# Kernel optimization log

Hardware: AMD Instinct MI355X
Metric: run time of the kernel (lower is better)

Reference implementation:

```python
import jax, jax.numpy as jnp
import numpy as np

EPS = 1e-5
NUM_HEADS = 16
HEAD_DIM = 64


def layernorm(x, g, b):
    mu = jnp.mean(x, axis=-1, keepdims=True)
    var = jnp.mean(jnp.square(x - mu), axis=-1, keepdims=True)
    return (x - mu) * jax.lax.rsqrt(var + EPS) * g + b


def setup_inputs() -> dict:
    key = jax.random.key(0)
    ks = jax.random.split(key, 10)
    B, S, Q, D = 4, 4096, 256, 1024
    x = jax.random.normal(ks[0], (B, S, D), dtype=jnp.float32)
    queries = jax.random.normal(ks[1], (B, Q, D), dtype=jnp.float32)
    attn_mask = jax.random.randint(ks[2], (B, NUM_HEADS, Q, S), 0, 2) == 1
    key_padding_mask = jax.random.randint(ks[3], (B, S), 0, 2) == 1
    scale = 1.0 / np.sqrt(2.0 * D)  # xavier-ish
    Wq = jax.random.normal(ks[4], (D, D), dtype=jnp.float32) * scale
    Wk = jax.random.normal(ks[5], (D, D), dtype=jnp.float32) * scale
    Wv = jax.random.normal(ks[6], (D, D), dtype=jnp.float32) * scale
    Wo = jax.random.normal(ks[7], (D, D), dtype=jnp.float32) * scale
    ln1_g = jnp.ones((D,), jnp.float32); ln1_b = jnp.zeros((D,), jnp.float32)
    ln2_g = jnp.ones((D,), jnp.float32); ln2_b = jnp.zeros((D,), jnp.float32)
    return {"x": x, "queries": queries, "attn_mask": attn_mask,
            "key_padding_mask": key_padding_mask, "Wq": Wq, "Wk": Wk,
            "Wv": Wv, "Wo": Wo, "ln1_g": ln1_g, "ln1_b": ln1_b,
            "ln2_g": ln2_g, "ln2_b": ln2_b}


def reference(x, queries, attn_mask, key_padding_mask, Wq, Wk, Wv, Wo,
              ln1_g, ln1_b, ln2_g, ln2_b):
    B, S, D = x.shape
    Q = queries.shape[1]
    H, hd = NUM_HEADS, HEAD_DIM

    xn = layernorm(x, ln1_g, ln1_b)
    q = (queries @ Wq.T).reshape(B, Q, H, hd)
    k = (xn @ Wk.T).reshape(B, S, H, hd)
    v = (xn @ Wv.T).reshape(B, S, H, hd)

    # scores: (B, H, Q, S)
    scores = jnp.einsum('bqhd,bshd->bhqs', q, k) / np.sqrt(hd)

    mask = attn_mask | key_padding_mask[:, None, None, :]
    neg_inf = jnp.float32(-jnp.inf)
    masked = jnp.where(mask, neg_inf, scores)
    all_masked = jnp.all(mask, axis=-1, keepdims=True)  # rows fully masked
    safe = jnp.where(all_masked, 0.0, masked)
    attn = jax.nn.softmax(safe, axis=-1)
    attn = jnp.where(all_masked, 0.0, attn)

    out = jnp.einsum('bhqs,bshd->bqhd', attn, v).reshape(B, Q, D)
    out = layernorm(out, ln2_g, ln2_b)
    return out @ Wo.T, attn.mean(axis=1)
```

## Files before the change

kernel.cpp:

```cpp
#include <hip/hip_runtime.h>
#include <math.h>

#define DEV __device__ __forceinline__

typedef float  f4v  __attribute__((ext_vector_type(4)));
typedef __bf16 b8v  __attribute__((ext_vector_type(8)));
typedef short  s8v  __attribute__((ext_vector_type(8)));

DEV short f2b(float f){ __bf16 h = (__bf16)f; return __builtin_bit_cast(short, h); }

DEV void gload16(const void* g, void* l){
  __builtin_amdgcn_global_load_lds((const __attribute__((address_space(1))) void*)g,
                                   (__attribute__((address_space(3))) void*)l, 16, 0, 0);
}

DEV b8v ldsf(const short* p){ return __builtin_bit_cast(b8v, *(const s8v*)p); }

DEV f4v mfma16(b8v a, b8v b, f4v c){ return __builtin_amdgcn_mfma_f32_16x16x32_bf16(a, b, c, 0, 0, 0); }

__global__ void cvt5_kernel(const float* __restrict__ s0, const float* __restrict__ s1,
                            const float* __restrict__ s2, const float* __restrict__ s3,
                            const float* __restrict__ s4,
                            short* __restrict__ d0, short* __restrict__ d1,
                            short* __restrict__ d2, short* __restrict__ d3,
                            short* __restrict__ d4){
  int i = blockIdx.x*256 + threadIdx.x;
  int buf = i >> 18, j = i & 262143;
  const float* s = (buf==0)?s0:(buf==1)?s1:(buf==2)?s2:(buf==3)?s3:s4;
  short*       d = (buf==0)?d0:(buf==1)?d1:(buf==2)?d2:(buf==3)?d3:d4;
  float4 v = ((const float4*)s)[j];
  ((short4*)d)[j] = make_short4(f2b(v.x), f2b(v.y), f2b(v.z), f2b(v.w));
}

__global__ __launch_bounds__(256) void ln_kernel(const float* __restrict__ x, const float* __restrict__ gg,
                                                 const float* __restrict__ bb, short* __restrict__ out){
  int row = blockIdx.x, tid = threadIdx.x;
  const float4 v = ((const float4*)(x + (size_t)row*1024))[tid];
  float s = v.x + v.y + v.z + v.w;
  #pragma unroll
  for (int off=1; off<64; off<<=1) s += __shfl_xor(s, off);
  __shared__ float red[4];
  if ((tid&63)==0) red[tid>>6] = s;
  __syncthreads();
  float mu = (red[0]+red[1]+red[2]+red[3]) * (1.0f/1024.0f);
  float d0=v.x-mu, d1=v.y-mu, d2=v.z-mu, d3=v.w-mu;
  float q = d0*d0 + d1*d1 + d2*d2 + d3*d3;
  #pragma unroll
  for (int off=1; off<64; off<<=1) q += __shfl_xor(q, off);
  __syncthreads();
  if ((tid&63)==0) red[tid>>6] = q;
  __syncthreads();
  float rs = rsqrtf((red[0]+red[1]+red[2]+red[3]) * (1.0f/1024.0f) + 1e-5f);
  float4 g4 = ((const float4*)gg)[tid];
  float4 b4 = ((const float4*)bb)[tid];
  short4 o = make_short4(f2b(d0*rs*g4.x + b4.x), f2b(d1*rs*g4.y + b4.y),
                         f2b(d2*rs*g4.z + b4.z), f2b(d3*rs*g4.w + b4.w));
  ((short4*)(out + (size_t)row*1024))[tid] = o;
}

__global__ __launch_bounds__(256) void ln_reduce_kernel(const float* __restrict__ opart, const float* __restrict__ gg,
                                                        const float* __restrict__ bb, short* __restrict__ out){
  int row = blockIdx.x, tid = threadIdx.x;
  float4 v = make_float4(0.f,0.f,0.f,0.f);
  #pragma unroll
  for (int sc=0; sc<16; ++sc){
    float4 t = ((const float4*)(opart + ((size_t)sc*1024 + row)*1024))[tid];
    v.x += t.x; v.y += t.y; v.z += t.z; v.w += t.w;
  }
  float s = v.x + v.y + v.z + v.w;
  #pragma unroll
  for (int off=1; off<64; off<<=1) s += __shfl_xor(s, off);
  __shared__ float red[4];
  if ((tid&63)==0) red[tid>>6] = s;
  __syncthreads();
  float mu = (red[0]+red[1]+red[2]+red[3]) * (1.0f/1024.0f);
  float d0=v.x-mu, d1=v.y-mu, d2=v.z-mu, d3=v.w-mu;
  float q = d0*d0 + d1*d1 + d2*d2 + d3*d3;
  #pragma unroll
  for (int off=1; off<64; off<<=1) q += __shfl_xor(q, off);
  __syncthreads();
  if ((tid&63)==0) red[tid>>6] = q;
  __syncthreads();
  float rs = rsqrtf((red[0]+red[1]+red[2]+red[3]) * (1.0f/1024.0f) + 1e-5f);
  float4 g4 = ((const float4*)gg)[tid];
  float4 b4 = ((const float4*)bb)[tid];
  short4 o = make_short4(f2b(d0*rs*g4.x + b4.x), f2b(d1*rs*g4.y + b4.y),
                         f2b(d2*rs*g4.z + b4.z), f2b(d3*rs*g4.w + b4.w));
  ((short4*)(out + (size_t)row*1024))[tid] = o;
}

template<int OUTF32>
__global__ __launch_bounds__(256,2) void gemm_bt(const short* __restrict__ A, const short* __restrict__ B,
                                                 void* __restrict__ C, int M, int N, int K){
  __shared__ short sA[128*32];
  __shared__ short sB[128*32];
  int tid=threadIdx.x, lane=tid&63, wv=tid>>6, g=lane>>4, r=lane&15;
  int wr=wv>>1, wc=wv&1;
  int m0=blockIdx.x*128, n0=blockIdx.y*128;
  f4v z = {0.f,0.f,0.f,0.f};
  f4v acc[4][4];
  #pragma unroll
  for (int i=0;i<4;++i){
    #pragma unroll
    for (int j=0;j<4;++j) acc[i][j]=z;
  }
  int nkt = K >> 5;
  for (int kt=0; kt<nkt; ++kt){
    __syncthreads();
    #pragma unroll
    for (int i=0;i<2;++i){
      int idx = i*256 + wv*64 + lane;
      int row = idx>>2, sl = idx&3;
      gload16(A + (size_t)(m0+row)*K + kt*32 + sl*8, &sA[(i*256+wv*64)*8]);
    }
    #pragma unroll
    for (int i=0;i<2;++i){
      int idx = i*256 + wv*64 + lane;
      int row = idx>>2, sl = idx&3;
      gload16(B + (size_t)(n0+row)*K + kt*32 + sl*8, &sB[(i*256+wv*64)*8]);
    }
    __syncthreads();
    b8v af[4], bf[4];
    #pragma unroll
    for (int mf=0;mf<4;++mf) af[mf] = ldsf(&sA[(wr*64+mf*16+r)*32 + g*8]);
    #pragma unroll
    for (int nf=0;nf<4;++nf) bf[nf] = ldsf(&sB[(wc*64+nf*16+r)*32 + g*8]);
    #pragma unroll
    for (int mf=0;mf<4;++mf){
      #pragma unroll
      for (int nf=0;nf<4;++nf)
        acc[mf][nf] = mfma16(af[mf], bf[nf], acc[mf][nf]);
    }
  }
  #pragma unroll
  for (int mf=0;mf<4;++mf){
    #pragma unroll
    for (int nf=0;nf<4;++nf){
      #pragma unroll
      for (int j=0;j<4;++j){
        int m = m0 + wr*64 + mf*16 + g*4 + j;
        int n = n0 + wc*64 + nf*16 + r;
        if (OUTF32) ((float*)C)[(size_t)m*N + n] = acc[mf][nf][j];
        else        ((short*)C)[(size_t)m*N + n] = f2b(acc[mf][nf][j]);
      }
    }
  }
}

__global__ __launch_bounds__(512,2) void gemm_dual_bt(const short* __restrict__ A, const short* __restrict__ B0,
                                                      const short* __restrict__ B1, short* __restrict__ C0,
                                                      short* __restrict__ C1, int M, int N, int K){
  __shared__ short sA[256*32];
  __shared__ short sB0[128*32];
  __shared__ short sB1[128*32];
  int tid=threadIdx.x, lane=tid&63, wv=tid>>6, g=lane>>4, r=lane&15;
  int wr=wv>>1, wc=wv&1;
  int m0=blockIdx.x*256, n0=blockIdx.y*128;
  f4v z = {0.f,0.f,0.f,0.f};
  f4v a0[4][4], a1[4][4];
  #pragma unroll
  for (int i=0;i<4;++i){
    #pragma unroll
    for (int j=0;j<4;++j){ a0[i][j]=z; a1[i][j]=z; }
  }
  int nkt = K >> 5;
  for (int kt=0; kt<nkt; ++kt){
    __syncthreads();
    #pragma unroll
    for (int i=0;i<2;++i){
      int idx = i*512 + tid;
      int row = idx>>2, sl = idx&3;
      gload16(A + (size_t)(m0+row)*K + kt*32 + sl*8, &sA[(i*512+wv*64)*8]);
    }
    {
      int row = tid>>2, sl = tid&3;
      gload16(B0 + (size_t)(n0+row)*K + kt*32 + sl*8, &sB0[(wv*64)*8]);
      gload16(B1 + (size_t)(n0+row)*K + kt*32 + sl*8, &sB1[(wv*64)*8]);
    }
    __syncthreads();
    b8v af[4], b0[4], b1[4];
    #pragma unroll
    for (int mf=0;mf<4;++mf) af[mf] = ldsf(&sA[(wr*64+mf*16+r)*32 + g*8]);
    #pragma unroll
    for (int nf=0;nf<4;++nf){
      b0[nf] = ldsf(&sB0[(wc*64+nf*16+r)*32 + g*8]);
      b1[nf] = ldsf(&sB1[(wc*64+nf*16+r)*32 + g*8]);
    }
    #pragma unroll
    for (int mf=0;mf<4;++mf){
      #pragma unroll
      for (int nf=0;nf<4;++nf){
        a0[mf][nf] = mfma16(af[mf], b0[nf], a0[mf][nf]);
        a1[mf][nf] = mfma16(af[mf], b1[nf], a1[mf][nf]);
      }
    }
  }
  #pragma unroll
  for (int mf=0;mf<4;++mf){
    #pragma unroll
    for (int nf=0;nf<4;++nf){
      #pragma unroll
      for (int j=0;j<4;++j){
        int m = m0 + wr*64 + mf*16 + g*4 + j;
        int n = n0 + wc*64 + nf*16 + r;
        C0[(size_t)m*N + n] = f2b(a0[mf][nf][j]);
        C1[(size_t)m*N + n] = f2b(a1[mf][nf][j]);
      }
    }
  }
}

__global__ __launch_bounds__(256) void vtrans_kernel(const short* __restrict__ v, short* __restrict__ vt){
  int bid = blockIdx.x;
  int sb = bid & 63, bh = bid >> 6;
  int b = bh >> 4, h = bh & 15;
  int s0 = sb*64;
  __shared__ short t[64][80];
  int tid = threadIdx.x;
  #pragma unroll
  for (int i=0;i<2;++i){
    int idx = tid + i*256;
    int row = idx>>3, sl = idx&7;
    *(s8v*)&t[row][sl*8] = *(const s8v*)(v + (size_t)(b*4096 + s0 + row)*1024 + h*64 + sl*8);
  }
  __syncthreads();
  int hd = tid>>2, part = tid&3;
  s8v o0, o1;
  #pragma unroll
  for (int j=0;j<8;++j){ o0[j] = t[part*16+j][hd]; o1[j] = t[part*16+8+j][hd]; }
  size_t base = (size_t)(bh*64+hd)*4096 + s0 + part*16;
  *(s8v*)(vt + base)     = o0;
  *(s8v*)(vt + base + 8) = o1;
}

__global__ __launch_bounds__(256,2) void lsum_kernel(const short* __restrict__ qp, const short* __restrict__ kb,
                                                     const int* __restrict__ am, const int* __restrict__ kpm,
                                                     unsigned* __restrict__ pm, float* __restrict__ lpart){
  int bid = blockIdx.x;
  int sc = bid & 15, bh = bid >> 4;
  int b = bh >> 4, h = bh & 15;
  int s0 = sc*256;
  __shared__ short sQ[256*64];
  __shared__ short sK[256*64];
  __shared__ unsigned sPM[256*8];
  __shared__ unsigned kw[8];
  int tid=threadIdx.x, lane=tid&63, wv=tid>>6, g=lane>>4, r=lane&15;

  #pragma unroll
  for (int i=0;i<8;++i){
    int idx = i*256 + wv*64 + lane;
    int row = idx>>3, cbs = (idx&7)^(row&7);
    gload16(qp + (size_t)(b*256 + row)*1024 + h*64 + cbs*8, &sQ[(i*256+wv*64)*8]);
  }
  #pragma unroll
  for (int i=0;i<8;++i){
    int idx = i*256 + wv*64 + lane;
    int row = idx>>3, cbs = (idx&7)^(row&7);
    gload16(kb + (size_t)(b*4096 + s0 + row)*1024 + h*64 + cbs*8, &sK[(i*256+wv*64)*8]);
  }
  if (tid < 8){
    unsigned bits = 0;
    const int4* kp = (const int4*)(kpm + (size_t)b*4096 + s0 + tid*32);
    #pragma unroll
    for (int j=0;j<8;++j){
      int4 t = kp[j];
      bits |= (unsigned)(t.x!=0) << (j*4+0);
      bits |= (unsigned)(t.y!=0) << (j*4+1);
      bits |= (unsigned)(t.z!=0) << (j*4+2);
      bits |= (unsigned)(t.w!=0) << (j*4+3);
    }
    kw[tid] = bits;
  }
  unsigned rowbits[8];
  const int4* ap = (const int4*)(am + (size_t)(bh*256 + tid)*4096 + s0);
  #pragma unroll
  for (int w=0;w<8;++w){
    unsigned bits = 0;
    #pragma unroll
    for (int j=0;j<8;++j){
      int4 t = ap[w*8+j];
      bits |= (unsigned)(t.x!=0) << (j*4+0);
      bits |= (unsigned)(t.y!=0) << (j*4+1);
      bits |= (unsigned)(t.z!=0) << (j*4+2);
      bits |= (unsigned)(t.w!=0) << (j*4+3);
    }
    rowbits[w] = bits;
  }
  __syncthreads();
  #pragma unroll
  for (int w=0;w<8;++w){
    unsigned mword = rowbits[w] | kw[w];
    sPM[tid*8+w] = mword;
    pm[(size_t)bid*2048 + tid*8 + w] = mword;
  }
  __syncthreads();

  b8v a[4][2];
  #pragma unroll
  for (int mf=0;mf<4;++mf){
    #pragma unroll
    for (int ks=0;ks<2;++ks){
      int q = wv*64 + mf*16 + r;
      a[mf][ks] = ldsf(&sQ[q*64 + (((ks*4+g)^(q&7))*8)]);
    }
  }
  float lacc[4][4];
  #pragma unroll
  for (int mf=0;mf<4;++mf){
    #pragma unroll
    for (int j=0;j<4;++j) lacc[mf][j] = 0.f;
  }
  f4v z = {0.f,0.f,0.f,0.f};
  #pragma unroll 4
  for (int nf=0;nf<16;++nf){
    int srow = nf*16 + r;
    b8v b0 = ldsf(&sK[srow*64 + ((g^(srow&7))*8)]);
    b8v b1 = ldsf(&sK[srow*64 + (((4+g)^(srow&7))*8)]);
    f4v acc[4];
    #pragma unroll
    for (int mf=0;mf<4;++mf){
      acc[mf] = mfma16(a[mf][0], b0, z);
      acc[mf] = mfma16(a[mf][1], b1, acc[mf]);
    }
    #pragma unroll
    for (int mf=0;mf<4;++mf){
      #pragma unroll
      for (int j=0;j<4;++j){
        int q = wv*64 + mf*16 + g*4 + j;
        unsigned wm = sPM[q*8 + (nf>>1)];
        bool mskd = (wm >> ((nf&1)*16 + r)) & 1u;
        lacc[mf][j] += mskd ? 0.f : __expf(acc[mf][j]*0.125f);
      }
    }
  }
  #pragma unroll
  for (int off=1; off<16; off<<=1){
    #pragma unroll
    for (int mf=0;mf<4;++mf){
      #pragma unroll
      for (int j=0;j<4;++j) lacc[mf][j] += __shfl_xor(lacc[mf][j], off);
    }
  }
  if (r == 0){
    #pragma unroll
    for (int mf=0;mf<4;++mf){
      #pragma unroll
      for (int j=0;j<4;++j){
        int q = wv*64 + mf*16 + g*4 + j;
        lpart[(size_t)bid*256 + q] = lacc[mf][j];
      }
    }
  }
}

__global__ void lcomb_kernel(const float* __restrict__ lpart, float* __restrict__ linv){
  int row = blockIdx.x*256 + threadIdx.x;
  int q = row & 255, bh = row >> 8;
  float l = 0.f;
  #pragma unroll
  for (int sc=0; sc<16; ++sc) l += lpart[(size_t)(bh*16+sc)*256 + q];
  linv[row] = (l > 0.f) ? (1.0f/l) : 0.f;
}

__global__ __launch_bounds__(512,2) void attn_pv_kernel(const short* __restrict__ qp, const short* __restrict__ kb,
                                                        const short* __restrict__ vt, const unsigned* __restrict__ pm,
                                                        const float* __restrict__ linv, float* __restrict__ opart,
                                                        float* __restrict__ out2){
  int bid = blockIdx.x;
  int sc = bid & 15, qt = (bid>>4)&3, b = bid>>6;
  int s0 = sc*256, q0 = qt*64;
  __shared__ short sK[256*64];
  __shared__ short sV[64*256];
  __shared__ short sQ[64*64];
  __shared__ unsigned sPM[64*8];
  int tid=threadIdx.x, lane=tid&63, wv=tid>>6, g=lane>>4, r=lane&15;
  int wq = wv>>2, ws = wv&3;
  f4v z = {0.f,0.f,0.f,0.f};
  float macc[2][4][4];
  #pragma unroll
  for (int mf=0;mf<2;++mf){
    #pragma unroll
    for (int nf=0;nf<4;++nf){
      #pragma unroll
      for (int j=0;j<4;++j) macc[mf][nf][j] = 0.f;
    }
  }

  for (int h=0; h<16; ++h){
    int bh = b*16 + h;
    __syncthreads();
    {
      int row = tid>>3, cbs = (tid&7)^(row&7);
      gload16(qp + (size_t)(b*256 + q0 + row)*1024 + h*64 + cbs*8, &sQ[(wv*64)*8]);
    }
    #pragma unroll
    for (int i=0;i<4;++i){
      int idx = i*512 + tid;
      int row = idx>>3, cbs = (idx&7)^(row&7);
      gload16(kb + (size_t)(b*4096 + s0 + row)*1024 + h*64 + cbs*8, &sK[(i*512+wv*64)*8]);
    }
    #pragma unroll
    for (int i=0;i<4;++i){
      int idx = i*512 + tid;
      int row = idx>>5, sl = idx&31, sls = sl^(row&7);
      gload16(vt + (size_t)(bh*64 + row)*4096 + s0 + sls*8, &sV[(i*512+wv*64)*8]);
    }
    {
      int row = tid>>3, w = tid&7;
      sPM[tid] = pm[(size_t)(bh*16+sc)*2048 + (q0+row)*8 + w];
    }
    __syncthreads();

    b8v aq[2][2];
    #pragma unroll
    for (int mf=0;mf<2;++mf){
      #pragma unroll
      for (int ks=0;ks<2;++ks){
        int qrow = wq*32 + mf*16 + r;
        aq[mf][ks] = ldsf(&sQ[qrow*64 + (((ks*4+g)^(qrow&7))*8)]);
      }
    }
    f4v accs[2][4];
    #pragma unroll
    for (int mf=0;mf<2;++mf){
      #pragma unroll
      for (int nf=0;nf<4;++nf) accs[mf][nf] = z;
    }
    #pragma unroll
    for (int nf=0;nf<4;++nf){
      int srow = ws*64 + nf*16 + r;
      b8v b0 = ldsf(&sK[srow*64 + ((g^(srow&7))*8)]);
      b8v b1 = ldsf(&sK[srow*64 + (((4+g)^(srow&7))*8)]);
      #pragma unroll
      for (int mf=0;mf<2;++mf){
        accs[mf][nf] = mfma16(aq[mf][0], b0, accs[mf][nf]);
        accs[mf][nf] = mfma16(aq[mf][1], b1, accs[mf][nf]);
      }
    }
    __syncthreads();

    #pragma unroll
    for (int mf=0;mf<2;++mf){
      #pragma unroll
      for (int j=0;j<4;++j){
        int ql = wq*32 + mf*16 + g*4 + j;
        float iv = linv[(size_t)bh*256 + q0 + ql];
        #pragma unroll
        for (int nf=0;nf<4;++nf){
          unsigned wm = sPM[ql*8 + ws*2 + (nf>>1)];
          bool mskd = (wm >> ((nf&1)*16 + r)) & 1u;
          float p = mskd ? 0.f : __expf(accs[mf][nf][j]*0.125f) * iv;
          macc[mf][nf][j] += p;
          int sl_ = ws*64 + nf*16 + r;
          sK[ql*256 + (((sl_>>3)^(ql&7))*8) + (sl_&7)] = f2b(p);
        }
      }
    }
    __syncthreads();

    f4v acco[2]; acco[0]=z; acco[1]=z;
    #pragma unroll
    for (int ks=0;ks<8;++ks){
      int vrow = ws*16 + r;
      b8v bv = ldsf(&sV[vrow*256 + (((ks*4+g)^(vrow&7))*8)]);
      #pragma unroll
      for (int mf=0;mf<2;++mf){
        int prow = wq*32 + mf*16 + r;
        b8v ap = ldsf(&sK[prow*256 + (((ks*4+g)^(prow&7))*8)]);
        acco[mf] = mfma16(ap, bv, acco[mf]);
      }
    }
    #pragma unroll
    for (int mf=0;mf<2;++mf){
      #pragma unroll
      for (int j=0;j<4;++j)
        opart[((size_t)sc*1024 + b*256 + q0 + wq*32 + mf*16 + g*4 + j)*1024 + h*64 + ws*16 + r] = acco[mf][j];
    }
  }

  #pragma unroll
  for (int mf=0;mf<2;++mf){
    #pragma unroll
    for (int nf=0;nf<4;++nf){
      #pragma unroll
      for (int j=0;j<4;++j){
        int q = q0 + wq*32 + mf*16 + g*4 + j;
        int s = s0 + ws*64 + nf*16 + r;
        out2[(size_t)(b*256 + q)*4096 + s] = macc[mf][nf][j] * 0.0625f;
      }
    }
  }
}

extern "C" void kernel_launch(void* const* d_in, const int* in_sizes, int n_in,
                              void* d_out, int out_size, void* d_ws, size_t ws_size,
                              hipStream_t stream){
  const float* x       = (const float*)d_in[0];
  const float* queries = (const float*)d_in[1];
  const int*   am      = (const int*)d_in[2];
  const int*   kpm     = (const int*)d_in[3];
  const float* Wq      = (const float*)d_in[4];
  const float* Wk      = (const float*)d_in[5];
  const float* Wv      = (const float*)d_in[6];
  const float* Wo      = (const float*)d_in[7];
  const float* ln1g    = (const float*)d_in[8];
  const float* ln1b    = (const float*)d_in[9];
  const float* ln2g    = (const float*)d_in[10];
  const float* ln2b    = (const float*)d_in[11];
  float* out0 = (float*)d_out;
  float* out2 = out0 + (size_t)4*256*1024;
  char* ws = (char*)d_ws;

  size_t off = 0;
  auto alloc = [&](size_t bytes){ void* p = ws + off; off += (bytes + 255) & ~(size_t)255; return p; };
  short*    xn   = (short*)alloc(33554432);
  short*    vt   = xn;
  short*    kb   = (short*)alloc(33554432);
  short*    vb   = (short*)alloc(33554432);
  short*    wqb  = (short*)alloc(2097152);
  short*    wkb  = (short*)alloc(2097152);
  short*    wvb  = (short*)alloc(2097152);
  short*    wob  = (short*)alloc(2097152);
  short*    qbf  = (short*)alloc(2097152);
  short*    qpj  = (short*)alloc(2097152);
  unsigned* pmw  = (unsigned*)alloc(8388608);
  float*    lpart= (float*)alloc(1048576);
  float*    linv = (float*)alloc(65536);
  float*    opart= (float*)alloc(67108864);
  short*    onb  = (short*)alloc(2097152);

  cvt5_kernel<<<5120,256,0,stream>>>(queries, Wq, Wk, Wv, Wo, qbf, wqb, wkb, wvb, wob);
  ln_kernel<<<16384,256,0,stream>>>(x, ln1g, ln1b, xn);
  gemm_dual_bt<<<dim3(64,8),512,0,stream>>>(xn, wkb, wvb, kb, vb, 16384, 1024, 1024);
  gemm_bt<0><<<dim3(8,8),256,0,stream>>>(qbf, wqb, qpj, 1024, 1024, 1024);
  vtrans_kernel<<<4096,256,0,stream>>>(vb, vt);
  lsum_kernel<<<1024,256,0,stream>>>(qpj, kb, am, kpm, pmw, lpart);
  lcomb_kernel<<<64,256,0,stream>>>(lpart, linv);
  attn_pv_kernel<<<256,512,0,stream>>>(qpj, kb, vt, pmw, linv, opart, out2);
  ln_reduce_kernel<<<1024,256,0,stream>>>(opart, ln2g, ln2b, onb);
  gemm_bt<1><<<dim3(8,8),256,0,stream>>>(onb, wob, out0, 1024, 1024, 1024);
}
```

Measured before the change: 383.9 us.

## Double-buffer GEMMs, shrink small GEMM tiles, store partial attention outputs in bf16

The large K/V dual GEMM now double-buffers its LDS tiles, prefetching the next k-slice while the current one is computed. That removes one barrier per iteration. The two 1024x1024 GEMMs get a new 64x64-tile kernel with a swizzled, double-buffered 64-wide k-slice, which launches 256 blocks instead of 64 to fill more CUs. Per-chunk attention partial outputs are stored as bf16 instead of fp32, halving that write/read traffic at some precision cost in the 16-way sum before LayerNorm. Doubling LDS in the dual GEMM may reduce occupancy.

```diff
diff --git a/kernel.cpp b/kernel.cpp
--- a/kernel.cpp
+++ b/kernel.cpp
@@ -8,6 +8,7 @@
 typedef short  s8v  __attribute__((ext_vector_type(8)));
 
 DEV short f2b(float f){ __bf16 h = (__bf16)f; return __builtin_bit_cast(short, h); }
+DEV float b2f(short s){ __bf16 h = __builtin_bit_cast(__bf16, s); return (float)h; }
 
 DEV void gload16(const void* g, void* l){
   __builtin_amdgcn_global_load_lds((const __attribute__((address_space(1))) void*)g,
@@ -58,23 +59,23 @@
   ((short4*)(out + (size_t)row*1024))[tid] = o;
 }
 
-__global__ __launch_bounds__(256) void ln_reduce_kernel(const float* __restrict__ opart, const float* __restrict__ gg,
+__global__ __launch_bounds__(256) void ln_reduce_kernel(const short* __restrict__ opart, const float* __restrict__ gg,
                                                         const float* __restrict__ bb, short* __restrict__ out){
   int row = blockIdx.x, tid = threadIdx.x;
-  float4 v = make_float4(0.f,0.f,0.f,0.f);
+  float a0=0.f, a1=0.f, a2=0.f, a3=0.f;
   #pragma unroll
   for (int sc=0; sc<16; ++sc){
-    float4 t = ((const float4*)(opart + ((size_t)sc*1024 + row)*1024))[tid];
-    v.x += t.x; v.y += t.y; v.z += t.z; v.w += t.w;
-  }
-  float s = v.x + v.y + v.z + v.w;
+    short4 t = ((const short4*)(opart + ((size_t)sc*1024 + row)*1024))[tid];
+    a0 += b2f(t.x); a1 += b2f(t.y); a2 += b2f(t.z); a3 += b2f(t.w);
+  }
+  float s = a0 + a1 + a2 + a3;
   #pragma unroll
   for (int off=1; off<64; off<<=1) s += __shfl_xor(s, off);
   __shared__ float red[4];
   if ((tid&63)==0) red[tid>>6] = s;
   __syncthreads();
   float mu = (red[0]+red[1]+red[2]+red[3]) * (1.0f/1024.0f);
-  float d0=v.x-mu, d1=v.y-mu, d2=v.z-mu, d3=v.w-mu;
+  float d0=a0-mu, d1=a1-mu, d2=a2-mu, d3=a3-mu;
   float q = d0*d0 + d1*d1 + d2*d2 + d3*d3;
   #pragma unroll
   for (int off=1; off<64; off<<=1) q += __shfl_xor(q, off);
@@ -90,56 +91,64 @@
 }
 
 template<int OUTF32>
-__global__ __launch_bounds__(256,2) void gemm_bt(const short* __restrict__ A, const short* __restrict__ B,
-                                                 void* __restrict__ C, int M, int N, int K){
-  __shared__ short sA[128*32];
-  __shared__ short sB[128*32];
+__global__ __launch_bounds__(256) void gemm_small(const short* __restrict__ A, const short* __restrict__ B,
+                                                  void* __restrict__ C, int M, int N, int K){
+  __shared__ short sA[2][64*64];
+  __shared__ short sB[2][64*64];
   int tid=threadIdx.x, lane=tid&63, wv=tid>>6, g=lane>>4, r=lane&15;
   int wr=wv>>1, wc=wv&1;
-  int m0=blockIdx.x*128, n0=blockIdx.y*128;
+  int m0=blockIdx.x*64, n0=blockIdx.y*64;
   f4v z = {0.f,0.f,0.f,0.f};
-  f4v acc[4][4];
-  #pragma unroll
-  for (int i=0;i<4;++i){
-    #pragma unroll
-    for (int j=0;j<4;++j) acc[i][j]=z;
-  }
-  int nkt = K >> 5;
+  f4v acc[2][2];
+  #pragma unroll
+  for (int i=0;i<2;++i){
+    #pragma unroll
+    for (int j=0;j<2;++j) acc[i][j]=z;
+  }
+  auto stage = [&](int buf, int kt){
+    #pragma unroll
+    for (int i=0;i<2;++i){
+      int idx = i*256 + tid;
+      int row = idx>>3, cbs = (idx&7)^(row&7);
+      gload16(A + (size_t)(m0+row)*K + kt*64 + cbs*8, &sA[buf][(i*256+wv*64)*8]);
+      gload16(B + (size_t)(n0+row)*K + kt*64 + cbs*8, &sB[buf][(i*256+wv*64)*8]);
+    }
+  };
+  int nkt = K >> 6;
+  stage(0, 0);
+  __syncthreads();
   for (int kt=0; kt<nkt; ++kt){
+    int cur = kt & 1;
+    if (kt+1 < nkt) stage(cur^1, kt+1);
+    b8v af[2][2], bf[2][2];
+    #pragma unroll
+    for (int mf=0;mf<2;++mf){
+      #pragma unroll
+      for (int ks=0;ks<2;++ks){
+        int ra = wr*32 + mf*16 + r;
+        int rb = wc*32 + mf*16 + r;
+        af[mf][ks] = ldsf(&sA[cur][ra*64 + (((ks*4+g)^(ra&7))*8)]);
+        bf[mf][ks] = ldsf(&sB[cur][rb*64 + (((ks*4+g)^(rb&7))*8)]);
+      }
+    }
+    #pragma unroll
+    for (int mf=0;mf<2;++mf){
+      #pragma unroll
+      for (int nf=0;nf<2;++nf){
+        acc[mf][nf] = mfma16(af[mf][0], bf[nf][0], acc[mf][nf]);
+        acc[mf][nf] = mfma16(af[mf][1], bf[nf][1], acc[mf][nf]);
+      }
+    }
     __syncthreads();
-    #pragma unroll
-    for (int i=0;i<2;++i){
-      int idx = i*256 + wv*64 + lane;
-      int row = idx>>2, sl = idx&3;
-      gload16(A + (size_t)(m0+row)*K + kt*32 + sl*8, &sA[(i*256+wv*64)*8]);
-    }
-    #pragma unroll
-    for (int i=0;i<2;++i){
-      int idx = i*256 + wv*64 + lane;
-      int row = idx>>2, sl = idx&3;
-      gload16(B + (size_t)(n0+row)*K + kt*32 + sl*8, &sB[(i*256+wv*64)*8]);
-    }
-    __syncthreads();
-    b8v af[4], bf[4];
-    #pragma unroll
-    for (int mf=0;mf<4;++mf) af[mf] = ldsf(&sA[(wr*64+mf*16+r)*32 + g*8]);
-    #pragma unroll
-    for (int nf=0;nf<4;++nf) bf[nf] = ldsf(&sB[(wc*64+nf*16+r)*32 + g*8]);
-    #pragma unroll
-    for (int mf=0;mf<4;++mf){
-      #pragma unroll
-      for (int nf=0;nf<4;++nf)
-        acc[mf][nf] = mfma16(af[mf], bf[nf], acc[mf][nf]);
-    }
-  }
-  #pragma unroll
-  for (int mf=0;mf<4;++mf){
-    #pragma unroll
-    for (int nf=0;nf<4;++nf){
+  }
+  #pragma unroll
+  for (int mf=0;mf<2;++mf){
+    #pragma unroll
+    for (int nf=0;nf<2;++nf){
       #pragma unroll
       for (int j=0;j<4;++j){
-        int m = m0 + wr*64 + mf*16 + g*4 + j;
-        int n = n0 + wc*64 + nf*16 + r;
+        int m = m0 + wr*32 + mf*16 + g*4 + j;
+        int n = n0 + wc*32 + nf*16 + r;
         if (OUTF32) ((float*)C)[(size_t)m*N + n] = acc[mf][nf][j];
         else        ((short*)C)[(size_t)m*N + n] = f2b(acc[mf][nf][j]);
       }
@@ -150,9 +159,9 @@
 __global__ __launch_bounds__(512,2) void gemm_dual_bt(const short* __restrict__ A, const short* __restrict__ B0,
                                                       const short* __restrict__ B1, short* __restrict__ C0,
                                                       short* __restrict__ C1, int M, int N, int K){
-  __shared__ short sA[256*32];
-  __shared__ short sB0[128*32];
-  __shared__ short sB1[128*32];
+  __shared__ short sA[2][256*32];
+  __shared__ short sB0[2][128*32];
+  __shared__ short sB1[2][128*32];
   int tid=threadIdx.x, lane=tid&63, wv=tid>>6, g=lane>>4, r=lane&15;
   int wr=wv>>1, wc=wv&1;
   int m0=blockIdx.x*256, n0=blockIdx.y*128;
@@ -163,37 +172,42 @@
     #pragma unroll
     for (int j=0;j<4;++j){ a0[i][j]=z; a1[i][j]=z; }
   }
-  int nkt = K >> 5;
-  for (int kt=0; kt<nkt; ++kt){
-    __syncthreads();
+  auto stage = [&](int buf, int kt){
     #pragma unroll
     for (int i=0;i<2;++i){
       int idx = i*512 + tid;
       int row = idx>>2, sl = idx&3;
-      gload16(A + (size_t)(m0+row)*K + kt*32 + sl*8, &sA[(i*512+wv*64)*8]);
+      gload16(A + (size_t)(m0+row)*K + kt*32 + sl*8, &sA[buf][(i*512+wv*64)*8]);
     }
     {
       int row = tid>>2, sl = tid&3;
-      gload16(B0 + (size_t)(n0+row)*K + kt*32 + sl*8, &sB0[(wv*64)*8]);
-      gload16(B1 + (size_t)(n0+row)*K + kt*32 + sl*8, &sB1[(wv*64)*8]);
+      gload16(B0 + (size_t)(n0+row)*K + kt*32 + sl*8, &sB0[buf][(wv*64)*8]);
+      gload16(B1 + (size_t)(n0+row)*K + kt*32 + sl*8, &sB1[buf][(wv*64)*8]);
+    }
+  };
+  int nkt = K >> 5;
+  stage(0, 0);
+  __syncthreads();
+  for (int kt=0; kt<nkt; ++kt){
+    int cur = kt & 1;
+    if (kt+1 < nkt) stage(cur^1, kt+1);
+    b8v af[4], b0f[4], b1f[4];
+    #pragma unroll
+    for (int mf=0;mf<4;++mf) af[mf] = ldsf(&sA[cur][(wr*64+mf*16+r)*32 + g*8]);
+    #pragma unroll
+    for (int nf=0;nf<4;++nf){
+      b0f[nf] = ldsf(&sB0[cur][(wc*64+nf*16+r)*32 + g*8]);
+      b1f[nf] = ldsf(&sB1[cur][(wc*64+nf*16+r)*32 + g*8]);
+    }
+    #pragma unroll
+    for (int mf=0;mf<4;++mf){
+      #pragma unroll
+      for (int nf=0;nf<4;++nf){
+        a0[mf][nf] = mfma16(af[mf], b0f[nf], a0[mf][nf]);
+        a1[mf][nf] = mfma16(af[mf], b1f[nf], a1[mf][nf]);
+      }
     }
     __syncthreads();
-    b8v af[4], b0[4], b1[4];
-    #pragma unroll
-    for (int mf=0;mf<4;++mf) af[mf] = ldsf(&sA[(wr*64+mf*16+r)*32 + g*8]);
-    #pragma unroll
-    for (int nf=0;nf<4;++nf){
-      b0[nf] = ldsf(&sB0[(wc*64+nf*16+r)*32 + g*8]);
-      b1[nf] = ldsf(&sB1[(wc*64+nf*16+r)*32 + g*8]);
-    }
-    #pragma unroll
-    for (int mf=0;mf<4;++mf){
-      #pragma unroll
-      for (int nf=0;nf<4;++nf){
-        a0[mf][nf] = mfma16(af[mf], b0[nf], a0[mf][nf]);
-        a1[mf][nf] = mfma16(af[mf], b1[nf], a1[mf][nf]);
-      }
-    }
   }
   #pragma unroll
   for (int mf=0;mf<4;++mf){
@@ -364,7 +378,7 @@
 
 __global__ __launch_bounds__(512,2) void attn_pv_kernel(const short* __restrict__ qp, const short* __restrict__ kb,
                                                         const short* __restrict__ vt, const unsigned* __restrict__ pm,
-                                                        const float* __restrict__ linv, float* __restrict__ opart,
+                                                        const float* __restrict__ linv, short* __restrict__ opart,
                                                         float* __restrict__ out2){
   int bid = blockIdx.x;
   int sc = bid & 15, qt = (bid>>4)&3, b = bid>>6;
@@ -474,7 +488,7 @@
     for (int mf=0;mf<2;++mf){
       #pragma unroll
       for (int j=0;j<4;++j)
-        opart[((size_t)sc*1024 + b*256 + q0 + wq*32 + mf*16 + g*4 + j)*1024 + h*64 + ws*16 + r] = acco[mf][j];
+        opart[((size_t)sc*1024 + b*256 + q0 + wq*32 + mf*16 + g*4 + j)*1024 + h*64 + ws*16 + r] = f2b(acco[mf][j]);
     }
   }
 
@@ -526,17 +540,17 @@
   unsigned* pmw  = (unsigned*)alloc(8388608);
   float*    lpart= (float*)alloc(1048576);
   float*    linv = (float*)alloc(65536);
-  float*    opart= (float*)alloc(67108864);
+  short*    opart= (short*)alloc(33554432);
   short*    onb  = (short*)alloc(2097152);
 
   cvt5_kernel<<<5120,256,0,stream>>>(queries, Wq, Wk, Wv, Wo, qbf, wqb, wkb, wvb, wob);
   ln_kernel<<<16384,256,0,stream>>>(x, ln1g, ln1b, xn);
   gemm_dual_bt<<<dim3(64,8),512,0,stream>>>(xn, wkb, wvb, kb, vb, 16384, 1024, 1024);
-  gemm_bt<0><<<dim3(8,8),256,0,stream>>>(qbf, wqb, qpj, 1024, 1024, 1024);
+  gemm_small<0><<<dim3(16,16),256,0,stream>>>(qbf, wqb, qpj, 1024, 1024, 1024);
   vtrans_kernel<<<4096,256,0,stream>>>(vb, vt);
   lsum_kernel<<<1024,256,0,stream>>>(qpj, kb, am, kpm, pmw, lpart);
   lcomb_kernel<<<64,256,0,stream>>>(lpart, linv);
   attn_pv_kernel<<<256,512,0,stream>>>(qpj, kb, vt, pmw, linv, opart, out2);
   ln_reduce_kernel<<<1024,256,0,stream>>>(opart, ln2g, ln2b, onb);
-  gemm_bt<1><<<dim3(8,8),256,0,stream>>>(onb, wob, out0, 1024, 1024, 1024);
-}
+  gemm_small<1><<<dim3(16,16),256,0,stream>>>(onb, wob, out0, 1024, 1024, 1024);
+}
```

New measurement: 340.1 us. 11.4% less time.
